# Kernel optimization log

Hardware: AMD Instinct MI355X
Metric: run time of the kernel (lower is better)

The kernel has to match this reference:

```python
import jax, jax.numpy as jnp
import numpy as np

B, T, C, H = 8, 1024, 768, 12
D = C // H  # head dim = 64

def setup_inputs() -> dict:
    key = jax.random.key(0)
    k0, k1, k2, k3, k4 = jax.random.split(key, 5)
    x = jax.random.normal(k0, (B, T, C), dtype=jnp.float32)
    # flax Dense params: kernel [in, out], bias [out]
    c_attn_kernel = jax.random.normal(k1, (C, 3 * C), dtype=jnp.float32) * (1.0 / np.sqrt(C))
    c_attn_bias = jax.random.normal(k2, (3 * C,), dtype=jnp.float32) * 0.01
    c_proj_kernel = jax.random.normal(k3, (C, C), dtype=jnp.float32) * (1.0 / np.sqrt(C))
    c_proj_bias = jax.random.normal(k4, (C,), dtype=jnp.float32) * 0.01
    return {"x": x, "c_attn_kernel": c_attn_kernel, "c_attn_bias": c_attn_bias,
            "c_proj_kernel": c_proj_kernel, "c_proj_bias": c_proj_bias}

def reference(x, c_attn_kernel, c_attn_bias, c_proj_kernel, c_proj_bias):
    Bc, Tc, Cc = x.shape
    qkv = x @ c_attn_kernel + c_attn_bias          # [B, T, 3C]
    q, k, v = jnp.split(qkv, 3, axis=-1)
    q = q.reshape(Bc, Tc, H, D).swapaxes(1, 2)     # [B, H, T, D]
    k = k.reshape(Bc, Tc, H, D).swapaxes(1, 2)
    v = v.reshape(Bc, Tc, H, D).swapaxes(1, 2)
    att = jnp.matmul(q, k.swapaxes(-2, -1)) * (1.0 / jnp.sqrt(jnp.float32(D)))  # [B, H, T, T]
    mask = jnp.tril(jnp.ones((Tc, Tc), dtype=bool)).reshape(1, 1, Tc, Tc)
    att = jnp.where(mask, att, -jnp.inf)
    att = jax.nn.softmax(att, axis=-1)
    # dropout=0.0 / train=False -> identity
    y = jnp.matmul(att, v)                          # [B, H, T, D]
    y = y.swapaxes(1, 2).reshape(Bc, Tc, Cc)        # [B, T, C]
    y = y @ c_proj_kernel + c_proj_bias
    return y
```

## Files before the change

### kernel.cpp

```cpp
#include <hip/hip_runtime.h>
#include <hip/hip_bf16.h>
#include <math.h>

#define BATCH 8
#define SEQ   1024
#define CH    768
#define NH    12
#define HD    64
#define HSZ   (BATCH * NH * SEQ * HD)

typedef __attribute__((ext_vector_type(8))) short short8;
typedef __attribute__((ext_vector_type(4))) short short4v;
typedef __attribute__((ext_vector_type(4))) float floatx4;

static __device__ inline short f2bf(float f) {
    union { float f; unsigned u; } x; x.f = f;
    unsigned r = (x.u + 0x7fffu + ((x.u >> 16) & 1u)) >> 16;
    return (short)r;
}

#define GLOAD_LDS16(g, l)                                                     \
    __builtin_amdgcn_global_load_lds(                                         \
        (const __attribute__((address_space(1))) void*)(g),                   \
        (__attribute__((address_space(3))) void*)(l), 16, 0, 0)

#define BARF()  do { asm volatile("" ::: "memory");                           \
                     __builtin_amdgcn_s_barrier();                            \
                     asm volatile("" ::: "memory"); } while (0)
#define LGKM0()  asm volatile("s_waitcnt lgkmcnt(0)" ::: "memory")
#define VMCNT(N) asm volatile("s_waitcnt vmcnt(" #N ")" ::: "memory")
#define SCHED0() __builtin_amdgcn_sched_barrier(0)

#define NCAST (BATCH * SEQ * CH / 1024)
#define NTA   ((3 * CH / 32) * (CH / 32))
#define NTP   ((CH / 32) * (CH / 32))

__device__ __forceinline__ void transpose_tile(
    const float* __restrict__ w, short* __restrict__ wt, int K, int N,
    int bx, int by, int tid, float (*tile)[33])
{
    const int tx = tid & 31, ty = tid >> 5;
    const int n0 = bx * 32, k0 = by * 32;
    #pragma unroll
    for (int i = 0; i < 4; i++)
        tile[ty + i * 8][tx] = w[(size_t)(k0 + ty + i * 8) * N + n0 + tx];
    __syncthreads();
    #pragma unroll
    for (int i = 0; i < 4; i++)
        wt[(size_t)(n0 + ty + i * 8) * K + k0 + tx] = f2bf(tile[tx][ty + i * 8]);
}

__global__ __launch_bounds__(256) void prep_kernel(
    const float* __restrict__ x, short* __restrict__ xb,
    const float* __restrict__ wa, short* __restrict__ wta,
    const float* __restrict__ wp, short* __restrict__ wtp)
{
    __shared__ float tile[32][33];
    const int bid = blockIdx.x, tid = threadIdx.x;
    if (bid < NCAST) {
        int i = (bid * 256 + tid) * 4;
        float4 v = *(const float4*)(x + i);
        short4v o = { f2bf(v.x), f2bf(v.y), f2bf(v.z), f2bf(v.w) };
        *(short4v*)(xb + i) = o;
    } else if (bid < NCAST + NTA) {
        int t = bid - NCAST;
        transpose_tile(wa, wta, CH, 3 * CH, t % (3 * CH / 32), t / (3 * CH / 32), tid, tile);
    } else {
        int t = bid - NCAST - NTA;
        transpose_tile(wp, wtp, CH, CH, t % (CH / 32), t / (CH / 32), tid, tile);
    }
}

__global__ __launch_bounds__(512, 2) void gemm1_8ph_kernel(
    const short* __restrict__ A, const short* __restrict__ Bt,
    const float* __restrict__ bias, short* __restrict__ qkv)
{
    const int K = CH;
    __shared__ __align__(16) short smem[57344];
    short* As = smem;
    short* Bs = smem + 32768;

    const int tid  = threadIdx.x;
    const int lane = tid & 63;
    const int col  = lane & 15;
    const int quad = lane >> 4;
    const int wave = tid >> 6;
    const int wm   = wave >> 2;
    const int wn   = wave & 3;

    const int bid = blockIdx.x;
    const int xcd = bid & 7;
    const int t8  = bid >> 3;
    const int mb  = xcd * 4 + t8 / 12;
    const int nb  = t8 % 12;
    const int m0  = mb * 256;
    const int n0  = nb * 192;

    const int srow = tid >> 3;
    const int swz  = ((tid & 7) ^ (srow & 7)) << 3;
    const short* aP[4];
    const short* bP[3];
    #pragma unroll
    for (int c = 0; c < 4; ++c)
        aP[c] = A + (size_t)(m0 + c * 64 + srow) * K + swz;
    #pragma unroll
    for (int c = 0; c < 3; ++c)
        bP[c] = Bt + (size_t)(n0 + c * 64 + srow) * K + swz;

    const int cswz0 = ((quad) ^ (col & 7)) << 3;
    const int cswz1 = cswz0 ^ 32;
    const int aBase = (wm * 128 + col) * 64;
    const int bBase = (wn * 48 + col) * 64;

    floatx4 acc[8][3];
    #pragma unroll
    for (int i = 0; i < 8; ++i)
        #pragma unroll
        for (int j = 0; j < 3; ++j)
            acc[i][j] = (floatx4){0.f, 0.f, 0.f, 0.f};

    GLOAD_LDS16(bP[0], &Bs[0 * 4096 + tid * 8]);
    GLOAD_LDS16(bP[1], &Bs[1 * 4096 + tid * 8]);
    GLOAD_LDS16(bP[2], &Bs[2 * 4096 + tid * 8]);
    GLOAD_LDS16(aP[0], &As[0 * 4096 + tid * 8]);
    GLOAD_LDS16(aP[2], &As[2 * 4096 + tid * 8]);
    GLOAD_LDS16(aP[1], &As[1 * 4096 + tid * 8]);
    GLOAD_LDS16(aP[3], &As[3 * 4096 + tid * 8]);
    VMCNT(2);
    BARF();

    #pragma unroll 1
    for (int t = 0; t < 12; ++t) {
        const int  P  = t & 1;
        const bool pf = (t < 11);
        const int  sk = (t + 1) * 64;
        const short* lA = As + P * 16384;
        const short* lB = Bs + P * 12288;
        short* wA = As + (P ^ 1) * 16384;
        short* wB = Bs + (P ^ 1) * 12288;

        short8 bf[3][2];
        #pragma unroll
        for (int nt = 0; nt < 3; ++nt) {
            bf[nt][0] = *(const short8*)&lB[bBase + nt * 1024 + cswz0];
            bf[nt][1] = *(const short8*)&lB[bBase + nt * 1024 + cswz1];
        }

        #pragma unroll
        for (int g = 0; g < 4; ++g) {
            short8 af[2][2];
            #pragma unroll
            for (int dm = 0; dm < 2; ++dm) {
                const int ro = aBase + (g * 2 + dm) * 1024;
                af[dm][0] = *(const short8*)&lA[ro + cswz0];
                af[dm][1] = *(const short8*)&lA[ro + cswz1];
            }
            if (g == 0 && pf) {
                GLOAD_LDS16(bP[0] + sk, &wB[0 * 4096 + tid * 8]);
                GLOAD_LDS16(bP[1] + sk, &wB[1 * 4096 + tid * 8]);
                GLOAD_LDS16(bP[2] + sk, &wB[2 * 4096 + tid * 8]);
            }
            if (g == 1 && pf) {
                GLOAD_LDS16(aP[0] + sk, &wA[0 * 4096 + tid * 8]);
                GLOAD_LDS16(aP[2] + sk, &wA[2 * 4096 + tid * 8]);
            }
            if (g == 2 && pf) {
                GLOAD_LDS16(aP[1] + sk, &wA[1 * 4096 + tid * 8]);
                GLOAD_LDS16(aP[3] + sk, &wA[3 * 4096 + tid * 8]);
            }
            BARF();
            LGKM0();
            SCHED0();
            __builtin_amdgcn_s_setprio(1);
            #pragma unroll
            for (int s = 0; s < 2; ++s)
                #pragma unroll
                for (int dm = 0; dm < 2; ++dm)
                    #pragma unroll
                    for (int nt = 0; nt < 3; ++nt)
                        acc[g * 2 + dm][nt] = __builtin_amdgcn_mfma_f32_16x16x32_bf16(
                            af[dm][s], bf[nt][s], acc[g * 2 + dm][nt], 0, 0, 0);
            __builtin_amdgcn_s_setprio(0);
            if (g == 1) {
                if (pf) { VMCNT(5); } else { VMCNT(0); }
            }
            if (g == 3 && pf) { VMCNT(2); }
            BARF();
        }
    }

    short* Es = smem;
    const int sel = nb >> 2;
    const int h0  = (nb & 3) * 3;
    const int bb  = m0 >> 10;
    const int t0  = m0 & 1023;

    if (sel < 2) {
        #pragma unroll
        for (int nt = 0; nt < 3; ++nt) {
            const int ln = wn * 48 + nt * 16 + col;
            const float bv = bias[n0 + ln];
            #pragma unroll
            for (int mt = 0; mt < 8; ++mt)
                #pragma unroll
                for (int r = 0; r < 4; ++r) {
                    const int lm = wm * 128 + mt * 16 + quad * 4 + r;
                    Es[lm * 200 + ln] = f2bf(acc[mt][nt][r] + bv);
                }
        }
        BARF();
        #pragma unroll
        for (int it = 0; it < 12; ++it) {
            const int id = it * 512 + tid;
            const int lm = id / 24, c24 = id - lm * 24;
            const int hp = c24 >> 3, dc = c24 & 7;
            short8 v = *(const short8*)&Es[lm * 200 + hp * 64 + dc * 8];
            size_t dst = (size_t)sel * HSZ +
                (((size_t)(bb * NH + h0 + hp)) * SEQ + t0 + lm) * HD + dc * 8;
            *(short8*)&qkv[dst] = v;
        }
    } else {
        #pragma unroll
        for (int nt = 0; nt < 3; ++nt) {
            const int ln = wn * 48 + nt * 16 + col;
            const float bv = bias[n0 + ln];
            #pragma unroll
            for (int mt = 0; mt < 8; ++mt) {
                const int lm = wm * 128 + mt * 16 + quad * 4;
                short4v pk;
                #pragma unroll
                for (int r = 0; r < 4; ++r) pk[r] = f2bf(acc[mt][nt][r] + bv);
                *(short4v*)&Es[ln * 264 + lm] = pk;
            }
        }
        BARF();
        #pragma unroll
        for (int it = 0; it < 12; ++it) {
            const int id = it * 512 + tid;
            const int ln = id >> 5, tc = id & 31;
            short8 v = *(const short8*)&Es[ln * 264 + tc * 8];
            const int hp = ln >> 6, d = ln & 63;
            size_t dst = (size_t)2 * HSZ +
                (((size_t)(bb * NH + h0 + hp)) * HD + d) * SEQ + t0 + tc * 8;
            *(short8*)&qkv[dst] = v;
        }
    }
}

template <int MODE, int BM, int BN, int NBLK, int MBX, int WPE>
__global__ __launch_bounds__(256, WPE) void gemm_bt_kernel(
    const short* __restrict__ A, const short* __restrict__ Bt,
    const float* __restrict__ bias, void* __restrict__ outv,
    int M, int N, int K)
{
    constexpr int MT  = BM / 32;
    constexpr int NT  = BN / 32;
    constexpr int ACH = BM / 64;
    constexpr int BCH = BN / 64;
    constexpr int STAGE_BYTES = (BM + BN) * 128;
    constexpr int EPI_BYTES   = (MODE == 1) ? (BN * 136 * 2) : 0;
    constexpr int LDS_BYTES   = STAGE_BYTES > EPI_BYTES ? STAGE_BYTES : EPI_BYTES;
    __shared__ __align__(16) char smem[LDS_BYTES];
    short* AsB = (short*)smem;
    short* BsB = (short*)(smem + BM * 128);

    const int tid  = threadIdx.x;
    const int lane = tid & 63;
    const int col  = lane & 15;
    const int quad = lane >> 4;
    const int wave = tid >> 6;
    const int wm = wave & 1, wn = wave >> 1;

    const int bid = blockIdx.x;
    const int j   = bid & 7;
    const int t   = bid >> 3;
    const int mb  = j * MBX + t / NBLK;
    const int nb  = t % NBLK;
    const int m0 = mb * BM, n0 = nb * BN;

    const int srow = tid >> 2;
    const int kc   = ((tid & 3) ^ (srow & 3)) * 8;
    const short* aptr[ACH];
    const short* bptr[BCH];
    #pragma unroll
    for (int c = 0; c < ACH; c++)
        aptr[c] = A + (size_t)(m0 + c * 64 + srow) * K + kc;
    #pragma unroll
    for (int c = 0; c < BCH; c++)
        bptr[c] = Bt + (size_t)(n0 + c * 64 + srow) * K + kc;

    floatx4 acc[MT][NT];
    #pragma unroll
    for (int i = 0; i < MT; i++)
        #pragma unroll
        for (int jj = 0; jj < NT; jj++)
            acc[i][jj] = (floatx4){0.f, 0.f, 0.f, 0.f};

    const int niter = K / 32;

    #pragma unroll
    for (int c = 0; c < ACH; c++) GLOAD_LDS16(aptr[c], &AsB[c * 2048 + tid * 8]);
    #pragma unroll
    for (int c = 0; c < BCH; c++) GLOAD_LDS16(bptr[c], &BsB[c * 2048 + tid * 8]);

    for (int k = 0; k < niter; k++) {
        __syncthreads();
        const int cur = k & 1, nxt = cur ^ 1;
        if (k + 1 < niter) {
            const int ko = (k + 1) * 32;
            #pragma unroll
            for (int c = 0; c < ACH; c++)
                GLOAD_LDS16(aptr[c] + ko, &AsB[nxt * BM * 32 + c * 2048 + tid * 8]);
            #pragma unroll
            for (int c = 0; c < BCH; c++)
                GLOAD_LDS16(bptr[c] + ko, &BsB[nxt * BN * 32 + c * 2048 + tid * 8]);
        }
        short8 af[MT], bf[NT];
        #pragma unroll
        for (int mt = 0; mt < MT; mt++) {
            const int row = wm * (BM / 2) + mt * 16 + col;
            af[mt] = *(const short8*)&AsB[cur * BM * 32 + row * 32 + ((quad ^ (row & 3)) << 3)];
        }
        #pragma unroll
        for (int nt = 0; nt < NT; nt++) {
            const int row = wn * (BN / 2) + nt * 16 + col;
            bf[nt] = *(const short8*)&BsB[cur * BN * 32 + row * 32 + ((quad ^ (row & 3)) << 3)];
        }
        #pragma unroll
        for (int mt = 0; mt < MT; mt++)
            #pragma unroll
            for (int nt = 0; nt < NT; nt++)
                acc[mt][nt] = __builtin_amdgcn_mfma_f32_16x16x32_bf16(
                    af[mt], bf[nt], acc[mt][nt], 0, 0, 0);
    }

    if constexpr (MODE == 0) {
        #pragma unroll
        for (int mt = 0; mt < MT; mt++) {
            #pragma unroll
            for (int r = 0; r < 4; r++) {
                const int m = m0 + wm * (BM / 2) + mt * 16 + quad * 4 + r;
                #pragma unroll
                for (int nt = 0; nt < NT; nt++) {
                    const int n = n0 + wn * (BN / 2) + nt * 16 + col;
                    ((float*)outv)[(size_t)m * N + n] = acc[mt][nt][r] + bias[n];
                }
            }
        }
    } else {
        __syncthreads();
        short* Es = (short*)smem;
        const int sel = n0 / CH;
        const int h0  = (n0 - sel * CH) >> 6;
        const int bb  = m0 >> 10;
        const int t0  = m0 & 1023;
        short* qkv = (short*)outv;

        if (sel < 2) {
            #pragma unroll
            for (int mt = 0; mt < MT; mt++)
                #pragma unroll
                for (int r = 0; r < 4; r++) {
                    const int lm = wm * (BM / 2) + mt * 16 + quad * 4 + r;
                    #pragma unroll
                    for (int nt = 0; nt < NT; nt++) {
                        const int ln = wn * (BN / 2) + nt * 16 + col;
                        Es[lm * 200 + ln] = f2bf(acc[mt][nt][r] + bias[n0 + ln]);
                    }
                }
            __syncthreads();
            #pragma unroll
            for (int it = 0; it < (BM * BN / 8) / 256; it++) {
                const int id = it * 256 + tid;
                const int hp = id >> 10, lm = (id >> 3) & 127, dc = id & 7;
                short8 v = *(const short8*)&Es[lm * 200 + hp * 64 + dc * 8];
                size_t dst = (size_t)sel * HSZ +
                    (((size_t)(bb * NH + h0 + hp)) * SEQ + t0 + lm) * HD + dc * 8;
                *(short8*)&qkv[dst] = v;
            }
        } else {
            #pragma unroll
            for (int nt = 0; nt < NT; nt++) {
                const int ln = wn * (BN / 2) + nt * 16 + col;
                const float bv = bias[n0 + ln];
                #pragma unroll
                for (int mt = 0; mt < MT; mt++) {
                    const int lm = wm * (BM / 2) + mt * 16 + quad * 4;
                    short4v pk;
                    #pragma unroll
                    for (int r = 0; r < 4; r++) pk[r] = f2bf(acc[mt][nt][r] + bv);
                    *(short4v*)&Es[ln * 136 + lm] = pk;
                }
            }
            __syncthreads();
            #pragma unroll
            for (int it = 0; it < (BM * BN / 8) / 256; it++) {
                const int id = it * 256 + tid;
                const int ln = id >> 4, tc = id & 15;
                short8 v = *(const short8*)&Es[ln * 136 + tc * 8];
                const int hp = ln >> 6, d = ln & 63;
                size_t dst = (size_t)2 * HSZ +
                    (((size_t)(bb * NH + h0 + hp)) * HD + d) * SEQ + t0 + tc * 8;
                *(short8*)&qkv[dst] = v;
            }
        }
    }
}

#define LDK 72

template <bool DIAG>
__device__ __forceinline__ void strip_step(
    const short* __restrict__ Ksh, const short* __restrict__ Vsh,
    short* __restrict__ pw, const short8* aq, floatx4* acc_o,
    floatx4& lacc, short8 bones, int col, int quad, int qrow0)
{
    floatx4 sacc[4];
    #pragma unroll
    for (int i = 0; i < 4; i++) sacc[i] = (floatx4){0.f, 0.f, 0.f, 0.f};
    #pragma unroll
    for (int s = 0; s < 2; s++)
        #pragma unroll
        for (int nt = 0; nt < 4; nt++) {
            short8 bk = *(const short8*)&Ksh[(nt * 16 + col) * LDK + s * 32 + quad * 8];
            sacc[nt] = __builtin_amdgcn_mfma_f32_16x16x32_bf16(aq[s], bk, sacc[nt], 0, 0, 0);
        }

    const float SCL = 0.18033688011112042f;
    #pragma unroll
    for (int r = 0; r < 4; r++)
        #pragma unroll
        for (int nt = 0; nt < 4; nt++) {
            float sv = sacc[nt][r] * SCL;
            if (DIAG && (nt * 16 + col) > (qrow0 + r)) sv = -INFINITY;
            float pv = __builtin_amdgcn_exp2f(sv);
            pw[(quad * 4 + r) * LDK + nt * 16 + col] =
                (short)(__builtin_bit_cast(unsigned, pv) >> 16);
        }
    __builtin_amdgcn_wave_barrier();

    short8 ap[2];
    ap[0] = *(const short8*)&pw[col * LDK + quad * 8];
    ap[1] = *(const short8*)&pw[col * LDK + 32 + quad * 8];

    #pragma unroll
    for (int s = 0; s < 2; s++) {
        #pragma unroll
        for (int nt = 0; nt < 4; nt++) {
            short8 bv = *(const short8*)&Vsh[(nt * 16 + col) * LDK + s * 32 + quad * 8];
            acc_o[nt] = __builtin_amdgcn_mfma_f32_16x16x32_bf16(ap[s], bv, acc_o[nt], 0, 0, 0);
        }
        lacc = __builtin_amdgcn_mfma_f32_16x16x32_bf16(ap[s], bones, lacc, 0, 0, 0);
    }
}

__global__ __launch_bounds__(256, 3) void attn_kernel(
    const short* __restrict__ Qg, const short* __restrict__ Kg,
    const short* __restrict__ Vg, short* __restrict__ Y)
{
    __shared__ __align__(16) short Ksh[64 * LDK];
    __shared__ __align__(16) short Vsh[64 * LDK];
    __shared__ __align__(16) short Psh[4][2][16 * LDK];

    const int tid  = threadIdx.x;
    const int wave = tid >> 6;
    const int lane = tid & 63;
    const int col  = lane & 15;
    const int quad = lane >> 4;
    const int bh = blockIdx.x;
    const int qt = 7 - blockIdx.y;
    const int b = bh / NH, h = bh - b * NH;

    const size_t kqbase = (size_t)bh * SEQ * HD;
    const size_t vbase  = (size_t)bh * HD * SEQ;

    short8 aq[2][2];
    #pragma unroll
    for (int st = 0; st < 2; st++) {
        const short* qp = Qg + kqbase +
            (size_t)(qt * 128 + st * 64 + wave * 16 + col) * HD + quad * 8;
        aq[st][0] = *(const short8*)(qp);
        aq[st][1] = *(const short8*)(qp + 32);
    }

    floatx4 acc_o[2][4];
    floatx4 lacc[2];
    #pragma unroll
    for (int st = 0; st < 2; st++) {
        lacc[st] = (floatx4){0.f, 0.f, 0.f, 0.f};
        #pragma unroll
        for (int i = 0; i < 4; i++) acc_o[st][i] = (floatx4){0.f, 0.f, 0.f, 0.f};
    }

    const short one_bf = (short)0x3F80;
    short8 bones = (col == 0)
        ? (short8){one_bf, one_bf, one_bf, one_bf, one_bf, one_bf, one_bf, one_bf}
        : (short8){0, 0, 0, 0, 0, 0, 0, 0};

    const int qrow0 = wave * 16 + quad * 4;

    const int idx0 = tid * 8, idx1 = (256 + tid) * 8;
    const int row0 = idx0 >> 6, offs0 = idx0 & 63;
    const int row1 = idx1 >> 6, offs1 = idx1 & 63;

    short8 kreg[2], vreg[2];
    {
        const short* ksrc = Kg + kqbase;
        const short* vsrc = Vg + vbase;
        kreg[0] = *(const short8*)&ksrc[idx0];
        kreg[1] = *(const short8*)&ksrc[idx1];
        vreg[0] = *(const short8*)&vsrc[(size_t)row0 * SEQ + offs0];
        vreg[1] = *(const short8*)&vsrc[(size_t)row1 * SEQ + offs1];
    }

    const int nkt = 2 * qt + 2;
    for (int kt = 0; kt < nkt; kt++) {
        __syncthreads();
        *(short8*)&Ksh[row0 * LDK + offs0] = kreg[0];
        *(short8*)&Ksh[row1 * LDK + offs1] = kreg[1];
        *(short8*)&Vsh[row0 * LDK + offs0] = vreg[0];
        *(short8*)&Vsh[row1 * LDK + offs1] = vreg[1];
        __syncthreads();

        if (kt + 1 < nkt) {
            const short* ksrc = Kg + kqbase + (size_t)(kt + 1) * 64 * HD;
            const short* vsrc = Vg + vbase + (kt + 1) * 64;
            kreg[0] = *(const short8*)&ksrc[idx0];
            kreg[1] = *(const short8*)&ksrc[idx1];
            vreg[0] = *(const short8*)&vsrc[(size_t)row0 * SEQ + offs0];
            vreg[1] = *(const short8*)&vsrc[(size_t)row1 * SEQ + offs1];
        }

        if (kt < 2 * qt) {
            strip_step<false>(Ksh, Vsh, Psh[wave][0], aq[0], acc_o[0], lacc[0],
                              bones, col, quad, qrow0);
            strip_step<false>(Ksh, Vsh, Psh[wave][1], aq[1], acc_o[1], lacc[1],
                              bones, col, quad, qrow0);
        } else if (kt == 2 * qt) {
            strip_step<true>(Ksh, Vsh, Psh[wave][0], aq[0], acc_o[0], lacc[0],
                             bones, col, quad, qrow0);
            strip_step<false>(Ksh, Vsh, Psh[wave][1], aq[1], acc_o[1], lacc[1],
                              bones, col, quad, qrow0);
        } else {
            strip_step<true>(Ksh, Vsh, Psh[wave][1], aq[1], acc_o[1], lacc[1],
                             bones, col, quad, qrow0);
        }
    }

    #pragma unroll
    for (int st = 0; st < 2; st++) {
        #pragma unroll
        for (int r = 0; r < 4; r++) {
            float l = __shfl(lacc[st][r], quad * 16, 64);
            float inv = 1.f / l;
            int t = qt * 128 + st * 64 + wave * 16 + quad * 4 + r;
            size_t ybase = ((size_t)(b * SEQ + t)) * CH + h * HD;
            #pragma unroll
            for (int nt = 0; nt < 4; nt++)
                Y[ybase + nt * 16 + col] = f2bf(acc_o[st][nt][r] * inv);
        }
    }
}

extern "C" void kernel_launch(void* const* d_in, const int* in_sizes, int n_in,
                              void* d_out, int out_size, void* d_ws, size_t ws_size,
                              hipStream_t stream)
{
    const float* x      = (const float*)d_in[0];
    const float* w_attn = (const float*)d_in[1];
    const float* b_attn = (const float*)d_in[2];
    const float* w_proj = (const float*)d_in[3];
    const float* b_proj = (const float*)d_in[4];
    float* out = (float*)d_out;

    short* qkv16 = (short*)d_ws;
    short* y16   = qkv16 + (size_t)3 * HSZ;
    short* xb    = y16   + (size_t)HSZ;
    short* wta   = xb    + (size_t)HSZ;
    short* wtp   = wta   + (size_t)3 * CH * CH;

    const int M = BATCH * SEQ;

    prep_kernel<<<NCAST + NTA + NTP, 256, 0, stream>>>(x, xb, w_attn, wta, w_proj, wtp);

    gemm1_8ph_kernel<<<384, 512, 0, stream>>>(xb, wta, b_attn, qkv16);

    dim3 ga(BATCH * NH, SEQ / 128);
    attn_kernel<<<ga, 256, 0, stream>>>(qkv16, qkv16 + (size_t)HSZ,
                                        qkv16 + (size_t)2 * HSZ, y16);

    gemm_bt_kernel<0, 64, 192, 4, 16, 4><<<512, 256, 0, stream>>>(
        y16, wtp, b_proj, out, M, CH, CH);
}
```

Before: 178.1 us.

## Single-buffer A tile in QKV GEMM to cut LDS and split epilogue staging

The QKV projection GEMM now keeps only one LDS buffer for the A operand and double-buffers only B. Its A chunks are reloaded in two halves, interleaved with compute, with tightened vmcnt waits. The epilogue stages output through LDS one wave-row half at a time, so it fits in the smaller buffer. The goal is to shrink shared memory per block (about 80KB) and allow higher occupancy. The cost is less prefetch slack and extra barriers, and the now-dead MODE 1 epilogue in the generic GEMM template is removed.

```diff
diff --git a/kernel.cpp b/kernel.cpp
--- a/kernel.cpp
+++ b/kernel.cpp
@@ -76,9 +76,9 @@
     const float* __restrict__ bias, short* __restrict__ qkv)
 {
     const int K = CH;
-    __shared__ __align__(16) short smem[57344];
+    __shared__ __align__(16) short smem[40960];
     short* As = smem;
-    short* Bs = smem + 32768;
+    short* Bb = smem + 16384;
 
     const int tid  = threadIdx.x;
     const int lane = tid & 63;
@@ -119,9 +119,9 @@
         for (int j = 0; j < 3; ++j)
             acc[i][j] = (floatx4){0.f, 0.f, 0.f, 0.f};
 
-    GLOAD_LDS16(bP[0], &Bs[0 * 4096 + tid * 8]);
-    GLOAD_LDS16(bP[1], &Bs[1 * 4096 + tid * 8]);
-    GLOAD_LDS16(bP[2], &Bs[2 * 4096 + tid * 8]);
+    GLOAD_LDS16(bP[0], &Bb[0 * 4096 + tid * 8]);
+    GLOAD_LDS16(bP[1], &Bb[1 * 4096 + tid * 8]);
+    GLOAD_LDS16(bP[2], &Bb[2 * 4096 + tid * 8]);
     GLOAD_LDS16(aP[0], &As[0 * 4096 + tid * 8]);
     GLOAD_LDS16(aP[2], &As[2 * 4096 + tid * 8]);
     GLOAD_LDS16(aP[1], &As[1 * 4096 + tid * 8]);
@@ -131,13 +131,12 @@
 
     #pragma unroll 1
     for (int t = 0; t < 12; ++t) {
-        const int  P  = t & 1;
-        const bool pf = (t < 11);
-        const int  sk = (t + 1) * 64;
-        const short* lA = As + P * 16384;
-        const short* lB = Bs + P * 12288;
-        short* wA = As + (P ^ 1) * 16384;
-        short* wB = Bs + (P ^ 1) * 12288;
+        const int  P   = t & 1;
+        const bool pf  = (t < 11);
+        const int  skc = t * 64;
+        const int  skn = (t + 1) * 64;
+        const short* lB = Bb + P * 12288;
+        short* wB = Bb + (P ^ 1) * 12288;
 
         short8 bf[3][2];
         #pragma unroll
@@ -152,21 +151,23 @@
             #pragma unroll
             for (int dm = 0; dm < 2; ++dm) {
                 const int ro = aBase + (g * 2 + dm) * 1024;
-                af[dm][0] = *(const short8*)&lA[ro + cswz0];
-                af[dm][1] = *(const short8*)&lA[ro + cswz1];
-            }
-            if (g == 0 && pf) {
-                GLOAD_LDS16(bP[0] + sk, &wB[0 * 4096 + tid * 8]);
-                GLOAD_LDS16(bP[1] + sk, &wB[1 * 4096 + tid * 8]);
-                GLOAD_LDS16(bP[2] + sk, &wB[2 * 4096 + tid * 8]);
-            }
-            if (g == 1 && pf) {
-                GLOAD_LDS16(aP[0] + sk, &wA[0 * 4096 + tid * 8]);
-                GLOAD_LDS16(aP[2] + sk, &wA[2 * 4096 + tid * 8]);
+                af[dm][0] = *(const short8*)&As[ro + cswz0];
+                af[dm][1] = *(const short8*)&As[ro + cswz1];
+            }
+            if (g == 0) {
+                if (t > 0) {
+                    GLOAD_LDS16(aP[1] + skc, &As[1 * 4096 + tid * 8]);
+                    GLOAD_LDS16(aP[3] + skc, &As[3 * 4096 + tid * 8]);
+                }
+                if (pf) {
+                    GLOAD_LDS16(bP[0] + skn, &wB[0 * 4096 + tid * 8]);
+                    GLOAD_LDS16(bP[1] + skn, &wB[1 * 4096 + tid * 8]);
+                    GLOAD_LDS16(bP[2] + skn, &wB[2 * 4096 + tid * 8]);
+                }
             }
             if (g == 2 && pf) {
-                GLOAD_LDS16(aP[1] + sk, &wA[1 * 4096 + tid * 8]);
-                GLOAD_LDS16(aP[3] + sk, &wA[3 * 4096 + tid * 8]);
+                GLOAD_LDS16(aP[0] + skn, &As[0 * 4096 + tid * 8]);
+                GLOAD_LDS16(aP[2] + skn, &As[2 * 4096 + tid * 8]);
             }
             BARF();
             LGKM0();
@@ -182,9 +183,9 @@
                             af[dm][s], bf[nt][s], acc[g * 2 + dm][nt], 0, 0, 0);
             __builtin_amdgcn_s_setprio(0);
             if (g == 1) {
-                if (pf) { VMCNT(5); } else { VMCNT(0); }
-            }
-            if (g == 3 && pf) { VMCNT(2); }
+                if (pf) { VMCNT(3); } else { VMCNT(0); }
+            }
+            if (g == 3 && pf) { VMCNT(0); }
             BARF();
         }
     }
@@ -197,52 +198,64 @@
 
     if (sel < 2) {
         #pragma unroll
-        for (int nt = 0; nt < 3; ++nt) {
-            const int ln = wn * 48 + nt * 16 + col;
-            const float bv = bias[n0 + ln];
-            #pragma unroll
-            for (int mt = 0; mt < 8; ++mt)
+        for (int half = 0; half < 2; ++half) {
+            if (half) BARF();
+            if (wm == half) {
                 #pragma unroll
-                for (int r = 0; r < 4; ++r) {
-                    const int lm = wm * 128 + mt * 16 + quad * 4 + r;
-                    Es[lm * 200 + ln] = f2bf(acc[mt][nt][r] + bv);
+                for (int nt = 0; nt < 3; ++nt) {
+                    const int ln = wn * 48 + nt * 16 + col;
+                    const float bv = bias[n0 + ln];
+                    #pragma unroll
+                    for (int mt = 0; mt < 8; ++mt)
+                        #pragma unroll
+                        for (int r = 0; r < 4; ++r) {
+                            const int lm = mt * 16 + quad * 4 + r;
+                            Es[lm * 200 + ln] = f2bf(acc[mt][nt][r] + bv);
+                        }
                 }
-        }
-        BARF();
-        #pragma unroll
-        for (int it = 0; it < 12; ++it) {
-            const int id = it * 512 + tid;
-            const int lm = id / 24, c24 = id - lm * 24;
-            const int hp = c24 >> 3, dc = c24 & 7;
-            short8 v = *(const short8*)&Es[lm * 200 + hp * 64 + dc * 8];
-            size_t dst = (size_t)sel * HSZ +
-                (((size_t)(bb * NH + h0 + hp)) * SEQ + t0 + lm) * HD + dc * 8;
-            *(short8*)&qkv[dst] = v;
+            }
+            BARF();
+            #pragma unroll
+            for (int it = 0; it < 6; ++it) {
+                const int id = it * 512 + tid;
+                const int lm = id / 24, c24 = id - lm * 24;
+                const int hp = c24 >> 3, dc = c24 & 7;
+                short8 v = *(const short8*)&Es[lm * 200 + hp * 64 + dc * 8];
+                size_t dst = (size_t)sel * HSZ +
+                    (((size_t)(bb * NH + h0 + hp)) * SEQ + t0 + half * 128 + lm) * HD + dc * 8;
+                *(short8*)&qkv[dst] = v;
+            }
         }
     } else {
         #pragma unroll
-        for (int nt = 0; nt < 3; ++nt) {
-            const int ln = wn * 48 + nt * 16 + col;
-            const float bv = bias[n0 + ln];
-            #pragma unroll
-            for (int mt = 0; mt < 8; ++mt) {
-                const int lm = wm * 128 + mt * 16 + quad * 4;
-                short4v pk;
+        for (int half = 0; half < 2; ++half) {
+            if (half) BARF();
+            if (wm == half) {
                 #pragma unroll
-                for (int r = 0; r < 4; ++r) pk[r] = f2bf(acc[mt][nt][r] + bv);
-                *(short4v*)&Es[ln * 264 + lm] = pk;
-            }
-        }
-        BARF();
-        #pragma unroll
-        for (int it = 0; it < 12; ++it) {
-            const int id = it * 512 + tid;
-            const int ln = id >> 5, tc = id & 31;
-            short8 v = *(const short8*)&Es[ln * 264 + tc * 8];
-            const int hp = ln >> 6, d = ln & 63;
-            size_t dst = (size_t)2 * HSZ +
-                (((size_t)(bb * NH + h0 + hp)) * HD + d) * SEQ + t0 + tc * 8;
-            *(short8*)&qkv[dst] = v;
+                for (int nt = 0; nt < 3; ++nt) {
+                    const int ln = wn * 48 + nt * 16 + col;
+                    const float bv = bias[n0 + ln];
+                    #pragma unroll
+                    for (int mt = 0; mt < 8; ++mt) {
+                        const int lm = mt * 16 + quad * 4;
+                        short4v pk;
+                        #pragma unroll
+                        for (int r = 0; r < 4; ++r) pk[r] = f2bf(acc[mt][nt][r] + bv);
+                        *(short4v*)&Es[ln * 136 + lm] = pk;
+                    }
+                }
+            }
+            BARF();
+            #pragma unroll
+            for (int it = 0; it < 6; ++it) {
+                const int id = it * 512 + tid;
+                const int ln = id >> 4, tc = id & 15;
+                short8 v = *(const short8*)&Es[ln * 136 + tc * 8];
+                const int hp = ln >> 6, d = ln & 63;
+                size_t dst = (size_t)2 * HSZ +
+                    (((size_t)(bb * NH + h0 + hp)) * HD + d) * SEQ + t0 + half * 128 + tc * 8;
+                *(short8*)&qkv[dst] = v;
+            }
         }
     }
 }
@@ -257,9 +270,7 @@
     constexpr int NT  = BN / 32;
     constexpr int ACH = BM / 64;
     constexpr int BCH = BN / 64;
-    constexpr int STAGE_BYTES = (BM + BN) * 128;
-    constexpr int EPI_BYTES   = (MODE == 1) ? (BN * 136 * 2) : 0;
-    constexpr int LDS_BYTES   = STAGE_BYTES > EPI_BYTES ? STAGE_BYTES : EPI_BYTES;
+    constexpr int LDS_BYTES = (BM + BN) * 128;
     __shared__ __align__(16) char smem[LDS_BYTES];
     short* AsB = (short*)smem;
     short* BsB = (short*)(smem + BM * 128);
@@ -334,74 +345,15 @@
                     af[mt], bf[nt], acc[mt][nt], 0, 0, 0);
     }
 
-    if constexpr (MODE == 0) {
-        #pragma unroll
-        for (int mt = 0; mt < MT; mt++) {
-            #pragma unroll
-            for (int r = 0; r < 4; r++) {
-                const int m = m0 + wm * (BM / 2) + mt * 16 + quad * 4 + r;
-                #pragma unroll
-                for (int nt = 0; nt < NT; nt++) {
-                    const int n = n0 + wn * (BN / 2) + nt * 16 + col;
-                    ((float*)outv)[(size_t)m * N + n] = acc[mt][nt][r] + bias[n];
-                }
-            }
-        }
-    } else {
-        __syncthreads();
-        short* Es = (short*)smem;
-        const int sel = n0 / CH;
-        const int h0  = (n0 - sel * CH) >> 6;
-        const int bb  = m0 >> 10;
-        const int t0  = m0 & 1023;
-        short* qkv = (short*)outv;
-
-        if (sel < 2) {
-            #pragma unroll
-            for (int mt = 0; mt < MT; mt++)
-                #pragma unroll
-                for (int r = 0; r < 4; r++) {
-                    const int lm = wm * (BM / 2) + mt * 16 + quad * 4 + r;
-                    #pragma unroll
-                    for (int nt = 0; nt < NT; nt++) {
-                        const int ln = wn * (BN / 2) + nt * 16 + col;
-                        Es[lm * 200 + ln] = f2bf(acc[mt][nt][r] + bias[n0 + ln]);
-                    }
-                }
-            __syncthreads();
-            #pragma unroll
-            for (int it = 0; it < (BM * BN / 8) / 256; it++) {
-                const int id = it * 256 + tid;
-                const int hp = id >> 10, lm = (id >> 3) & 127, dc = id & 7;
-                short8 v = *(const short8*)&Es[lm * 200 + hp * 64 + dc * 8];
-                size_t dst = (size_t)sel * HSZ +
-                    (((size_t)(bb * NH + h0 + hp)) * SEQ + t0 + lm) * HD + dc * 8;
-                *(short8*)&qkv[dst] = v;
-            }
-        } else {
+    #pragma unroll
+    for (int mt = 0; mt < MT; mt++) {
+        #pragma unroll
+        for (int r = 0; r < 4; r++) {
+            const int m = m0 + wm * (BM / 2) + mt * 16 + quad * 4 + r;
             #pragma unroll
             for (int nt = 0; nt < NT; nt++) {
-                const int ln = wn * (BN / 2) + nt * 16 + col;
-                const float bv = bias[n0 + ln];
-                #pragma unroll
-                for (int mt = 0; mt < MT; mt++) {
-                    const int lm = wm * (BM / 2) + mt * 16 + quad * 4;
-                    short4v pk;
-                    #pragma unroll
-                    for (int r = 0; r < 4; r++) pk[r] = f2bf(acc[mt][nt][r] + bv);
-                    *(short4v*)&Es[ln * 136 + lm] = pk;
-                }
-            }
-            __syncthreads();
-            #pragma unroll
-            for (int it = 0; it < (BM * BN / 8) / 256; it++) {
-                const int id = it * 256 + tid;
-                const int ln = id >> 4, tc = id & 15;
-                short8 v = *(const short8*)&Es[ln * 136 + tc * 8];
-                const int hp = ln >> 6, d = ln & 63;
-                size_t dst = (size_t)2 * HSZ +
-                    (((size_t)(bb * NH + h0 + hp)) * HD + d) * SEQ + t0 + tc * 8;
-                *(short8*)&qkv[dst] = v;
+                const int n = n0 + wn * (BN / 2) + nt * 16 + col;
+                ((float*)outv)[(size_t)m * N + n] = acc[mt][nt][r] + bias[n];
             }
         }
     }
```

Result: no change. 176.9 us (-0.7%).
